# Kernel tuning notes

Hardware: AMD Instinct MI355X
Metric: run time of the kernel (lower is better)

The kernel has to match this reference:

```python
import jax, jax.numpy as jnp
import numpy as np

T, N, DEG = 8, 8192, 15
H = 4


def _gat(x, src, dst, wl, wr, a, b):
    """GATv2Conv with concat=False (heads averaged). x: [N, Cin] -> [N, Cout].
    e_ij = a_h . LeakyReLU(Wl x_j + Wr x_i); softmax over incoming edges of i;
    messages are Wl x_j (PyG GATv2 convention, self-loops already in edge list)."""
    n = x.shape[0]
    h, c = a.shape
    gl = (x @ wl).reshape(n, h, c)  # source-side transform
    gr = (x @ wr).reshape(n, h, c)  # target-side transform
    z = jax.nn.leaky_relu(gl[src] + gr[dst], 0.2)          # [E,H,C]
    e = jnp.einsum('ehc,hc->eh', z, a)                     # [E,H]
    m = jax.ops.segment_max(e, dst, num_segments=n)        # [N,H]
    ex = jnp.exp(e - m[dst])
    den = jax.ops.segment_sum(ex, dst, num_segments=n)     # [N,H]
    msg = jax.ops.segment_sum(ex[:, :, None] * gl[src], dst, num_segments=n)
    return (msg / den[:, :, None]).mean(axis=1) + b


def _d3(x, esrc, edst, wl, wr, a, b):
    # spatio-temporal graph conv: GATv2 applied independently per timestep
    return jax.lax.map(lambda args: _gat(args[0], args[1], args[2], wl, wr, a, b),
                       (x, esrc, edst))


def setup_inputs() -> dict:
    key = jax.random.key(0)
    ks = iter(jax.random.split(key, 32))
    x = jax.random.normal(next(ks), (T, N, 64), dtype=jnp.float32)
    # fixed-degree random graph per timestep + self loops (PyG add_self_loops=True)
    dst_base = jnp.repeat(jnp.arange(N, dtype=jnp.int32), DEG)
    src_r = jax.random.randint(next(ks), (T, N * DEG), 0, N, dtype=jnp.int32)
    loop = jnp.arange(N, dtype=jnp.int32)
    edge_src = jnp.concatenate([src_r, jnp.broadcast_to(loop, (T, N))], axis=1)
    edge_dst = jnp.concatenate([jnp.broadcast_to(dst_base, (T, N * DEG)),
                                jnp.broadcast_to(loop, (T, N))], axis=1)

    def gat_p(k, cin, cout):
        k1, k2, k3 = jax.random.split(k, 3)
        s = 1.0 / np.sqrt(cin)
        return ((jax.random.normal(k1, (cin, H * cout)) * s).astype(jnp.float32),
                (jax.random.normal(k2, (cin, H * cout)) * s).astype(jnp.float32),
                (jax.random.normal(k3, (H, cout)) * s).astype(jnp.float32),
                jnp.zeros((cout,), jnp.float32))

    inp = {"x": x, "edge_src": edge_src, "edge_dst": edge_dst}
    for name, cin, cout in [("c1", 64, 128), ("c2", 128, 64), ("c3", 64, 64), ("c4", 128, 64),
                            ("r11", 64, 64), ("r12", 64, 64), ("r2", 128, 128),
                            ("f11", 64, 64), ("f2", 128, 128)]:
        wl, wr, a, b = gat_p(next(ks), cin, cout)
        inp[name + "_wl"], inp[name + "_wr"], inp[name + "_a"], inp[name + "_b"] = wl, wr, a, b
    # ConvTranspose1d(k=1) == per-node linear conv_ch -> in_channels; then Linear in_channels -> original_dim
    for name, cin, cout in [("r3", 128, 64), ("f3", 128, 64), ("r4", 64, 64), ("f4", 64, 64)]:
        inp[name + "_w"] = (jax.random.normal(next(ks), (cin, cout)) * (1.0 / np.sqrt(cin))).astype(jnp.float32)
        inp[name + "_b"] = jnp.zeros((cout,), jnp.float32)
    return inp


def reference(x, edge_src, edge_dst,
              c1_wl, c1_wr, c1_a, c1_b, c2_wl, c2_wr, c2_a, c2_b,
              c3_wl, c3_wr, c3_a, c3_b, c4_wl, c4_wr, c4_a, c4_b,
              r11_wl, r11_wr, r11_a, r11_b, r12_wl, r12_wr, r12_a, r12_b,
              r2_wl, r2_wr, r2_a, r2_b, r3_w, r3_b, r4_w, r4_b,
              f11_wl, f11_wr, f11_a, f11_b, f2_wl, f2_wr, f2_a, f2_b,
              f3_w, f3_b, f4_w, f4_b):
    elu = jax.nn.elu
    out = elu(_d3(x, edge_src, edge_dst, c1_wl, c1_wr, c1_a, c1_b))           # [T,N,128]
    emb = elu(_d3(out, edge_src, edge_dst, c2_wl, c2_wr, c2_a, c2_b))         # [T,N,64]
    emb = elu(jnp.concatenate([_d3(emb, edge_src, edge_dst, c3_wl, c3_wr, c3_a, c3_b), emb], -1))  # [T,N,128]
    emb = elu(_d3(emb, edge_src, edge_dst, c4_wl, c4_wr, c4_a, c4_b))         # [T,N,64]

    # reconstruction branch on edges at t = -1
    s1, d1 = edge_src[-1], edge_dst[-1]
    r = elu(_gat(emb[-1], s1, d1, r11_wl, r11_wr, r11_a, r11_b))
    r = elu(jnp.concatenate([_gat(r, s1, d1, r12_wl, r12_wr, r12_a, r12_b), r], -1))  # [N,128]
    # F.dropout in eval mode -> identity
    r = elu(_gat(r, s1, d1, r2_wl, r2_wr, r2_a, r2_b))
    r = jnp.tanh(r @ r3_w + r3_b)
    recon = r @ r4_w + r4_b

    # forecasting branch on edges at t = -2 (original reuses reconstruct12 here)
    s2, d2 = edge_src[-2], edge_dst[-2]
    f = elu(_gat(emb[-2], s2, d2, f11_wl, f11_wr, f11_a, f11_b))
    f = elu(jnp.concatenate([_gat(f, s2, d2, r12_wl, r12_wr, r12_a, r12_b), f], -1))
    f = elu(_gat(f, s2, d2, f2_wl, f2_wr, f2_a, f2_b))
    f = jnp.tanh(f @ f3_w + f3_b)
    forecast = f @ f4_w + f4_b
    return (recon, forecast, emb)
```

## Files before the change

kernel.cpp:

```cpp
#include <hip/hip_runtime.h>
#include <cmath>

constexpr int T_   = 8;
constexpr int N_   = 8192;
constexpr int DEG_ = 15;
constexpr int E_   = N_ * (DEG_ + 1);
constexpr float L2E_ = 1.44269504f;

__device__ __forceinline__ float elu1(float v) {
  return v > 0.f ? v : exp2f(v * L2E_) - 1.f;
}

typedef __attribute__((ext_vector_type(8))) short bf16x8;
typedef __attribute__((ext_vector_type(4))) float f32x4;

__device__ __forceinline__ ushort f2bf(float x) {
  uint u = __float_as_uint(x);
  return (ushort)((u + 0x7FFFu + ((u >> 16) & 1u)) >> 16);
}
__device__ __forceinline__ float bf2f(ushort h) {
  return __uint_as_float(((uint)h) << 16);
}

template<int CTRL>
__device__ __forceinline__ float dpp_add(float x) {
  const int t = __builtin_amdgcn_mov_dpp(__float_as_int(x), CTRL, 0xf, 0xf, true);
  return x + __int_as_float(t);
}
__device__ __forceinline__ float row_reduce16(float x) {
  x = dpp_add<0x121>(x);
  x = dpp_add<0x122>(x);
  x = dpp_add<0x124>(x);
  x = dpp_add<0x128>(x);
  return x;
}

__global__ __launch_bounds__(256) void pad_edges(
    const int* __restrict__ es, uint* __restrict__ es16, int total)
{
  const int idx = blockIdx.x * 256 + threadIdx.x;
  if (idx >= total) return;
  const int t = idx >> 13, i = idx & (N_ - 1);
  const int* e = es + (size_t)t * E_ + (size_t)i * DEG_;
  uint o[16];
  #pragma unroll
  for (int k = 0; k < DEG_; k++) o[k] = (uint)e[k];
  o[15] = (uint)i;
  uint4* dst = (uint4*)(es16 + (size_t)idx * 16);
  dst[0] = make_uint4(o[0], o[1], o[2], o[3]);
  dst[1] = make_uint4(o[4], o[5], o[6], o[7]);
  dst[2] = make_uint4(o[8], o[9], o[10], o[11]);
  dst[3] = make_uint4(o[12], o[13], o[14], o[15]);
}

__global__ __launch_bounds__(256) void split_x(
    const float* __restrict__ X, ushort* __restrict__ XH, ushort* __restrict__ XL, int n4)
{
  const int i = blockIdx.x * 256 + threadIdx.x;
  if (i >= n4) return;
  const float4 v = ((const float4*)X)[i];
  const ushort h0 = f2bf(v.x), h1 = f2bf(v.y), h2 = f2bf(v.z), h3 = f2bf(v.w);
  ushort4 hh; hh.x = h0; hh.y = h1; hh.z = h2; hh.w = h3;
  ushort4 ll;
  ll.x = f2bf(v.x - bf2f(h0)); ll.y = f2bf(v.y - bf2f(h1));
  ll.z = f2bf(v.z - bf2f(h2)); ll.w = f2bf(v.w - bf2f(h3));
  ((ushort4*)XH)[i] = hh;
  ((ushort4*)XL)[i] = ll;
}

struct WTable {
  const float* wl[9]; const float* wr[9];
  int lgK[9]; int lgHC[9]; int off[9];
};
__global__ __launch_bounds__(256) void split_wt_all(
    WTable tb, ushort* __restrict__ WH, ushort* __restrict__ WL)
{
  const int y = blockIdx.y;
  const int lgK = tb.lgK[y], lgHC = tb.lgHC[y];
  const int n2 = 2 << (lgK + lgHC);
  const int idx = blockIdx.x * 256 + threadIdx.x;
  if (idx >= n2) return;
  const int k = idx & ((1 << lgK) - 1);
  const int n = (idx >> lgK) & ((1 << lgHC) - 1);
  const int s = idx >> (lgK + lgHC);
  const float* W = s ? tb.wr[y] : tb.wl[y];
  const float v = W[((size_t)k << lgHC) + n];
  const ushort h = f2bf(v);
  WH[tb.off[y] + idx] = h;
  WL[tb.off[y] + idx] = f2bf(v - bf2f(h));
}

__global__ __launch_bounds__(256) void gemm_mfma(
    const ushort* __restrict__ Ah, const ushort* __restrict__ Al,
    const ushort* __restrict__ Wh, const ushort* __restrict__ Wl,
    float* __restrict__ Cl, float* __restrict__ Cr,
    int M, int Ncol, int K, int nt)
{
  __shared__ alignas(16) ushort lAh[4 * 1032];
  __shared__ alignas(16) ushort lAl[4 * 1032];
  __shared__ alignas(16) ushort lBh[4 * 520];
  __shared__ alignas(16) ushort lBl[4 * 520];

  const int z = blockIdx.z;
  const int t = (z < nt) ? z : z - nt;
  const int side = (z < nt) ? 0 : 1;
  const ushort* __restrict__ Bh = Wh + (size_t)side * Ncol * K;
  const ushort* __restrict__ Bl = Wl + (size_t)side * Ncol * K;
  float* __restrict__ C = (side ? Cr : Cl) + (size_t)t * M * Ncol;
  const size_t aoff = (size_t)t * M * K;

  const int bm = blockIdx.x * 128, bn = blockIdx.y * 64;
  const int tid = threadIdx.x;
  const int wid = tid >> 6, lane = tid & 63;
  const int l15 = lane & 15, lk = lane >> 4;

  f32x4 acc[2][4] = {};

  for (int k0 = 0; k0 < K; k0 += 32) {
    #pragma unroll
    for (int c = 0; c < 2; c++) {
      const int ch = tid + c * 256;
      const int row = ch >> 2, kc = ch & 3;
      const size_t ga = aoff + (size_t)(bm + row) * K + (k0 + kc * 8);
      *(uint4*)&lAh[kc * 1032 + row * 8] = *(const uint4*)(Ah + ga);
      *(uint4*)&lAl[kc * 1032 + row * 8] = *(const uint4*)(Al + ga);
    }
    {
      const int col = tid >> 2, kc = tid & 3;
      const size_t gb = (size_t)(bn + col) * K + (k0 + kc * 8);
      *(uint4*)&lBh[kc * 520 + col * 8] = *(const uint4*)(Bh + gb);
      *(uint4*)&lBl[kc * 520 + col * 8] = *(const uint4*)(Bl + gb);
    }
    __syncthreads();

    bf16x8 ah[2], al[2], bh4[4], bl4[4];
    const int r0 = wid * 32;
    #pragma unroll
    for (int rf = 0; rf < 2; rf++) {
      const int ro = (r0 + rf * 16 + l15) * 8;
      ah[rf] = *(const bf16x8*)&lAh[lk * 1032 + ro];
      al[rf] = *(const bf16x8*)&lAl[lk * 1032 + ro];
    }
    #pragma unroll
    for (int cf = 0; cf < 4; cf++) {
      const int co = (cf * 16 + l15) * 8;
      bh4[cf] = *(const bf16x8*)&lBh[lk * 520 + co];
      bl4[cf] = *(const bf16x8*)&lBl[lk * 520 + co];
    }
    #pragma unroll
    for (int rf = 0; rf < 2; rf++)
      #pragma unroll
      for (int cf = 0; cf < 4; cf++) {
        acc[rf][cf] = __builtin_amdgcn_mfma_f32_16x16x32_bf16(ah[rf], bh4[cf], acc[rf][cf], 0, 0, 0);
        acc[rf][cf] = __builtin_amdgcn_mfma_f32_16x16x32_bf16(ah[rf], bl4[cf], acc[rf][cf], 0, 0, 0);
        acc[rf][cf] = __builtin_amdgcn_mfma_f32_16x16x32_bf16(al[rf], bh4[cf], acc[rf][cf], 0, 0, 0);
      }
    __syncthreads();
  }

  #pragma unroll
  for (int rf = 0; rf < 2; rf++)
    #pragma unroll
    for (int cf = 0; cf < 4; cf++) {
      const int col = bn + cf * 16 + l15;
      #pragma unroll
      for (int reg = 0; reg < 4; reg++) {
        const int row = bm + wid * 32 + rf * 16 + lk * 4 + reg;
        C[(size_t)row * Ncol + col] = acc[rf][cf][reg];
      }
    }
}

template<int EPI>
__global__ __launch_bounds__(256) void gemm_k(
    const float* __restrict__ A, const float* __restrict__ B,
    float* __restrict__ C, const float* __restrict__ bias,
    int M, int Ncol, int K)
{
  __shared__ float As[16][68];
  __shared__ float Bs[16][64];

  const int tid = threadIdx.x;
  const int tx = tid & 15, ty = tid >> 4;
  const int bm = blockIdx.x * 64, bn = blockIdx.y * 64;

  const int arow = tid >> 2;
  const int akc  = (tid & 3) * 4;
  const int brow = tid >> 4;
  const int bc4  = (tid & 15) * 4;

  float acc[4][4];
  #pragma unroll
  for (int i = 0; i < 4; i++)
    #pragma unroll
    for (int j = 0; j < 4; j++) acc[i][j] = 0.f;

  for (int k0 = 0; k0 < K; k0 += 16) {
    const float4 va = *(const float4*)(A + (size_t)(bm + arow) * K + (k0 + akc));
    const float4 vb = *(const float4*)(B + (size_t)(k0 + brow) * Ncol + (bn + bc4));
    As[akc + 0][arow] = va.x; As[akc + 1][arow] = va.y;
    As[akc + 2][arow] = va.z; As[akc + 3][arow] = va.w;
    *(float4*)&Bs[brow][bc4] = vb;
    __syncthreads();
    #pragma unroll
    for (int kk = 0; kk < 16; kk++) {
      const float4 av = *(const float4*)&As[kk][ty * 4];
      const float4 bv = *(const float4*)&Bs[kk][tx * 4];
      const float a4[4] = {av.x, av.y, av.z, av.w};
      const float b4[4] = {bv.x, bv.y, bv.z, bv.w};
      #pragma unroll
      for (int i = 0; i < 4; i++)
        #pragma unroll
        for (int j = 0; j < 4; j++)
          acc[i][j] = fmaf(a4[i], b4[j], acc[i][j]);
    }
    __syncthreads();
  }

  #pragma unroll
  for (int i = 0; i < 4; i++) {
    const int row = bm + ty * 4 + i;
    const int col = bn + tx * 4;
    float v[4] = {acc[i][0], acc[i][1], acc[i][2], acc[i][3]};
    #pragma unroll
    for (int j = 0; j < 4; j++) v[j] += bias[col + j];
    if (EPI == 1) {
      #pragma unroll
      for (int j = 0; j < 4; j++) v[j] = tanhf(v[j]);
    }
    *(float4*)(C + (size_t)row * Ncol + col) = make_float4(v[0], v[1], v[2], v[3]);
  }
}

template<bool SWZ, bool CONCAT, bool WF32>
__global__ __launch_bounds__(256) void gat_agg256(
    const float* __restrict__ GL, const float* __restrict__ GR,
    const float* __restrict__ aw_, const float* __restrict__ bias,
    const uint* __restrict__ es16, float* __restrict__ out,
    const float* __restrict__ csrc,
    ushort* __restrict__ SHo, ushort* __restrict__ SLo)
{
  constexpr int C = 64;
  constexpr int OSTR = CONCAT ? 128 : 64;

  const int lane = threadIdx.x & 63;
  const int wid  = threadIdx.x >> 6;
  const int bid  = blockIdx.x;
  const int t    = SWZ ? (bid & 7) : 0;
  const int ib   = SWZ ? (bid >> 3) : bid;
  const int gid  = t * N_ + ib * 4 + wid;

  const float* __restrict__ gl = GL + (size_t)t * N_ * 256;
  const uint*  __restrict__ ep = es16 + (size_t)gid * 16;
  const uint lo16 = (uint)lane << 4;

  float gr[4], a6[4], a4c[4];
  {
    const float4 gv = *(const float4*)(GR + (size_t)gid * 256 + lane * 4);
    const float4 av = *(const float4*)(aw_ + lane * 4);
    gr[0] = gv.x; gr[1] = gv.y; gr[2] = gv.z; gr[3] = gv.w;
    a6[0] = 0.6f * L2E_ * av.x; a6[1] = 0.6f * L2E_ * av.y;
    a6[2] = 0.6f * L2E_ * av.z; a6[3] = 0.6f * L2E_ * av.w;
    a4c[0] = 0.4f * L2E_ * av.x; a4c[1] = 0.4f * L2E_ * av.y;
    a4c[2] = 0.4f * L2E_ * av.z; a4c[3] = 0.4f * L2E_ * av.w;
  }

  float acc[4] = {0.f, 0.f, 0.f, 0.f};
  float den = 0.f, m = 0.f;

  #pragma unroll
  for (int b = 0; b < 4; b++) {
    const uint4 j4 = *(const uint4*)(ep + b * 4);
    uint off[4];
    off[0] = (j4.x << 10) + lo16;
    off[1] = (j4.y << 10) + lo16;
    off[2] = (j4.z << 10) + lo16;
    off[3] = (j4.w << 10) + lo16;
    float g[4][4];
    #pragma unroll
    for (int q = 0; q < 4; q++) {
      const float4 v = *(const float4*)((const char*)gl + off[q]);
      g[q][0] = v.x; g[q][1] = v.y; g[q][2] = v.z; g[q][3] = v.w;
    }
    float p[4];
    #pragma unroll
    for (int q = 0; q < 4; q++) {
      float s = 0.f;
      #pragma unroll
      for (int u = 0; u < 4; u++) {
        const float z = g[q][u] + gr[u];
        s = fmaf(z, a6[u], s);
        s = fmaf(fabsf(z), a4c[u], s);
      }
      p[q] = s;
    }
    #pragma unroll
    for (int q = 0; q < 4; q++) p[q] = row_reduce16(p[q]);

    const float bmax = fmaxf(fmaxf(p[0], p[1]), fmaxf(p[2], p[3]));
    if (b == 0) {
      m = bmax;
    } else {
      const float nm = fmaxf(m, bmax);
      const float sc = exp2f(m - nm);
      den *= sc;
      #pragma unroll
      for (int u = 0; u < 4; u++) acc[u] *= sc;
      m = nm;
    }
    #pragma unroll
    for (int q = 0; q < 4; q++) {
      const float w = exp2f(p[q] - m);
      den += w;
      #pragma unroll
      for (int u = 0; u < 4; u++) acc[u] = fmaf(w, g[q][u], acc[u]);
    }
  }

  const float inv = 0.25f / den;
  #pragma unroll
  for (int u = 0; u < 4; u++) acc[u] *= inv;
  #pragma unroll
  for (int u = 0; u < 4; u++) {
    acc[u] += __shfl_xor(acc[u], 16);
    acc[u] += __shfl_xor(acc[u], 32);
  }

  if (lane < 16) {
    float o[4];
    #pragma unroll
    for (int u = 0; u < 4; u++)
      o[u] = elu1(acc[u] + bias[lane * 4 + u]);
    if (WF32)
      *(float4*)(out + (size_t)gid * OSTR + lane * 4) = make_float4(o[0], o[1], o[2], o[3]);
    ushort4 hh, ll;
    hh.x = f2bf(o[0]); hh.y = f2bf(o[1]); hh.z = f2bf(o[2]); hh.w = f2bf(o[3]);
    ll.x = f2bf(o[0] - bf2f(hh.x)); ll.y = f2bf(o[1] - bf2f(hh.y));
    ll.z = f2bf(o[2] - bf2f(hh.z)); ll.w = f2bf(o[3] - bf2f(hh.w));
    *(ushort4*)(SHo + (size_t)gid * OSTR + lane * 4) = hh;
    *(ushort4*)(SLo + (size_t)gid * OSTR + lane * 4) = ll;
  } else if (CONCAT && lane < 32) {
    const int q = lane - 16;
    const float4 v = *(const float4*)(csrc + (size_t)gid * C + q * 4);
    const float o0 = elu1(v.x), o1 = elu1(v.y), o2 = elu1(v.z), o3 = elu1(v.w);
    if (WF32)
      *(float4*)(out + (size_t)gid * OSTR + C + q * 4) = make_float4(o0, o1, o2, o3);
    ushort4 hh, ll;
    hh.x = f2bf(o0); hh.y = f2bf(o1); hh.z = f2bf(o2); hh.w = f2bf(o3);
    ll.x = f2bf(o0 - bf2f(hh.x)); ll.y = f2bf(o1 - bf2f(hh.y));
    ll.z = f2bf(o2 - bf2f(hh.z)); ll.w = f2bf(o3 - bf2f(hh.w));
    *(ushort4*)(SHo + (size_t)gid * OSTR + C + q * 4) = hh;
    *(ushort4*)(SLo + (size_t)gid * OSTR + C + q * 4) = ll;
  }
}

template<bool SWZ, bool WF32, bool SPLIT>
__global__ __launch_bounds__(256) void gat_agg512(
    const float* __restrict__ GL, const float* __restrict__ GR,
    const float* __restrict__ aw_, const float* __restrict__ bias,
    const uint* __restrict__ es16, float* __restrict__ out,
    ushort* __restrict__ SHo, ushort* __restrict__ SLo)
{
  __shared__ float smem[4][128];

  const int lane = threadIdx.x & 63;
  const int h    = threadIdx.x >> 6;
  const int bid  = blockIdx.x;
  int t, i;
  if (SWZ) {
    const int xcd = bid & 7;
    t = xcd >> 1;
    i = ((bid >> 3) << 1) | (xcd & 1);
  } else {
    t = 0; i = bid;
  }
  const int gid = t * N_ + i;

  const float* __restrict__ gl = GL + (size_t)t * N_ * 512;
  const uint*  __restrict__ ep = es16 + (size_t)gid * 16;
  const int cb = h * 128 + lane * 2;
  const uint cbo = (uint)cb << 2;

  float gr0, gr1, a60, a61, a40, a41;
  {
    const float2 gv = *(const float2*)(GR + (size_t)gid * 512 + cb);
    const float2 av = *(const float2*)(aw_ + cb);
    gr0 = gv.x; gr1 = gv.y;
    a60 = 0.6f * L2E_ * av.x; a61 = 0.6f * L2E_ * av.y;
    a40 = 0.4f * L2E_ * av.x; a41 = 0.4f * L2E_ * av.y;
  }

  float acc0 = 0.f, acc1 = 0.f, den = 0.f, m = 0.f;

  #pragma unroll
  for (int b = 0; b < 4; b++) {
    const uint4 j4 = *(const uint4*)(ep + b * 4);
    uint off[4];
    off[0] = (j4.x << 11) + cbo;
    off[1] = (j4.y << 11) + cbo;
    off[2] = (j4.z << 11) + cbo;
    off[3] = (j4.w << 11) + cbo;
    float g[4][2];
    #pragma unroll
    for (int q = 0; q < 4; q++) {
      const float2 v = *(const float2*)((const char*)gl + off[q]);
      g[q][0] = v.x; g[q][1] = v.y;
    }
    float p[4];
    #pragma unroll
    for (int q = 0; q < 4; q++) {
      const float z0 = g[q][0] + gr0;
      const float z1 = g[q][1] + gr1;
      float s = z0 * a60;
      s = fmaf(fabsf(z0), a40, s);
      s = fmaf(z1, a61, s);
      s = fmaf(fabsf(z1), a41, s);
      p[q] = s;
    }
    #pragma unroll
    for (int q = 0; q < 4; q++) {
      p[q] = row_reduce16(p[q]);
      p[q] += __shfl_xor(p[q], 16);
      p[q] += __shfl_xor(p[q], 32);
    }
    const float bmax = fmaxf(fmaxf(p[0], p[1]), fmaxf(p[2], p[3]));
    if (b == 0) {
      m = bmax;
    } else {
      const float nm = fmaxf(m, bmax);
      const float sc = exp2f(m - nm);
      den *= sc; acc0 *= sc; acc1 *= sc;
      m = nm;
    }
    #pragma unroll
    for (int q = 0; q < 4; q++) {
      const float w = exp2f(p[q] - m);
      den += w;
      acc0 = fmaf(w, g[q][0], acc0);
      acc1 = fmaf(w, g[q][1], acc1);
    }
  }

  const float inv = 0.25f / den;
  smem[h][lane * 2]     = acc0 * inv;
  smem[h][lane * 2 + 1] = acc1 * inv;
  __syncthreads();

  if (h == 0) {
    const int c = lane * 2;
    float s0 = smem[0][c] + smem[1][c] + smem[2][c] + smem[3][c];
    float s1 = smem[0][c + 1] + smem[1][c + 1] + smem[2][c + 1] + smem[3][c + 1];
    s0 = elu1(s0 + bias[c]);
    s1 = elu1(s1 + bias[c + 1]);
    if (WF32)
      *(float2*)(out + (size_t)gid * 128 + c) = make_float2(s0, s1);
    if (SPLIT) {
      ushort2 hh, ll;
      hh.x = f2bf(s0); hh.y = f2bf(s1);
      ll.x = f2bf(s0 - bf2f(hh.x)); ll.y = f2bf(s1 - bf2f(hh.y));
      *(ushort2*)(SHo + (size_t)gid * 128 + c) = hh;
      *(ushort2*)(SLo + (size_t)gid * 128 + c) = ll;
    }
  }
}

extern "C" void kernel_launch(void* const* d_in, const int* in_sizes, int n_in,
                              void* d_out, int out_size, void* d_ws, size_t ws_size,
                              hipStream_t stream)
{
  (void)in_sizes; (void)n_in; (void)out_size; (void)ws_size;

  const float* x  = (const float*)d_in[0];
  const int*   es = (const int*)d_in[1];
  const float *c1_wl=(const float*)d_in[3], *c1_wr=(const float*)d_in[4], *c1_a=(const float*)d_in[5], *c1_b=(const float*)d_in[6];
  const float *c2_wl=(const float*)d_in[7], *c2_wr=(const float*)d_in[8], *c2_a=(const float*)d_in[9], *c2_b=(const float*)d_in[10];
  const float *c3_wl=(const float*)d_in[11],*c3_wr=(const float*)d_in[12],*c3_a=(const float*)d_in[13],*c3_b=(const float*)d_in[14];
  const float *c4_wl=(const float*)d_in[15],*c4_wr=(const float*)d_in[16],*c4_a=(const float*)d_in[17],*c4_b=(const float*)d_in[18];
  const float *r11_wl=(const float*)d_in[19],*r11_wr=(const float*)d_in[20],*r11_a=(const float*)d_in[21],*r11_b=(const float*)d_in[22];
  const float *r12_wl=(const float*)d_in[23],*r12_wr=(const float*)d_in[24],*r12_a=(const float*)d_in[25],*r12_b=(const float*)d_in[26];
  const float *r2_wl=(const float*)d_in[27],*r2_wr=(const float*)d_in[28],*r2_a=(const float*)d_in[29],*r2_b=(const float*)d_in[30];
  const float *f11_wl=(const float*)d_in[31],*f11_wr=(const float*)d_in[32],*f11_a=(const float*)d_in[33],*f11_b=(const float*)d_in[34];
  const float *f2_wl=(const float*)d_in[35],*f2_wr=(const float*)d_in[36],*f2_a=(const float*)d_in[37],*f2_b=(const float*)d_in[38];
  const float *r3_w=(const float*)d_in[39], *r3_b=(const float*)d_in[40];
  const float *f3_w=(const float*)d_in[41], *f3_b=(const float*)d_in[42];
  const float *r4_w=(const float*)d_in[43], *r4_b=(const float*)d_in[44];
  const float *f4_w=(const float*)d_in[45], *f4_b=(const float*)d_in[46];

  float* ws = (float*)d_ws;
  float* GL = ws;
  float* GR = GL + (size_t)16777216;
  float* A1 = GR + (size_t)16777216;
  float* B0 = A1 + (size_t)T_ * N_ * 64;
  float* B1 = B0 + (size_t)N_ * 128;
  ushort* SH  = (ushort*)(B1 + (size_t)N_ * 128);
  ushort* SL  = SH + (size_t)8388608;
  ushort* SH2 = SL + (size_t)8388608;
  ushort* SL2 = SH2 + (size_t)8388608;
  ushort* WH  = SL2 + (size_t)8388608;
  ushort* WL  = WH + (size_t)589824;
  uint*  ES16 = (uint*)(WL + (size_t)589824);

  float* recon = (float*)d_out;
  float* fcst  = recon + (size_t)N_ * 64;
  float* emb   = fcst + (size_t)N_ * 64;

  const dim3 blk(256);

  pad_edges<<<dim3(T_ * N_ / 256), blk, 0, stream>>>(es, ES16, T_ * N_);
  split_x<<<dim3(T_ * N_ * 64 / 4 / 256), blk, 0, stream>>>(x, SH, SL, T_ * N_ * 64 / 4);
  WTable tb;
  const float* wls[9] = {c1_wl, c2_wl, c3_wl, c4_wl, r11_wl, r12_wl, r2_wl, f11_wl, f2_wl};
  const float* wrs[9] = {c1_wr, c2_wr, c3_wr, c4_wr, r11_wr, r12_wr, r2_wr, f11_wr, f2_wr};
  const int Ks[9]  = {64, 128, 64, 128, 64, 64, 128, 64, 128};
  const int HCs[9] = {512, 256, 256, 256, 256, 256, 512, 256, 512};
  int woff[9]; int acc_off = 0;
  for (int y = 0; y < 9; y++) {
    tb.wl[y] = wls[y]; tb.wr[y] = wrs[y];
    tb.lgK[y] = __builtin_ctz(Ks[y]); tb.lgHC[y] = __builtin_ctz(HCs[y]);
    woff[y] = acc_off; tb.off[y] = acc_off;
    acc_off += 2 * Ks[y] * HCs[y];
  }
  split_wt_all<<<dim3(512, 9), blk, 0, stream>>>(tb, WH, WL);

  for (int ch = 0; ch < 2; ch++) {
    const int t0 = ch * 4, nt = 4;
    gemm_mfma<<<dim3(N_ / 128, 8, 2 * nt), blk, 0, stream>>>(
        SH + (size_t)t0 * N_ * 64, SL + (size_t)t0 * N_ * 64,
        WH + woff[0], WL + woff[0], GL, GR, N_, 512, 64, nt);
    gat_agg512<true, false, true><<<dim3(nt * N_), blk, 0, stream>>>(
        GL, GR, c1_a, c1_b, ES16 + (size_t)t0 * N_ * 16, nullptr,
        SH2 + (size_t)t0 * N_ * 128, SL2 + (size_t)t0 * N_ * 128);
  }
  gemm_mfma<<<dim3(N_ / 128, 4, 2 * T_), blk, 0, stream>>>(
      SH2, SL2, WH + woff[1], WL + woff[1], GL, GR, N_, 256, 128, T_);
  gat_agg256<true, false, true><<<dim3(T_ * N_ / 4), blk, 0, stream>>>(
      GL, GR, c2_a, c2_b, ES16, A1, nullptr, SH, SL);
  gemm_mfma<<<dim3(N_ / 128, 4, 2 * T_), blk, 0, stream>>>(
      SH, SL, WH + woff[2], WL + woff[2], GL, GR, N_, 256, 64, T_);
  gat_agg256<true, true, false><<<dim3(T_ * N_ / 4), blk, 0, stream>>>(
      GL, GR, c3_a, c3_b, ES16, nullptr, A1, SH, SL);
  gemm_mfma<<<dim3(N_ / 128, 4, 2 * T_), blk, 0, stream>>>(
      SH, SL, WH + woff[3], WL + woff[3], GL, GR, N_, 256, 128, T_);
  gat_agg256<true, false, true><<<dim3(T_ * N_ / 4), blk, 0, stream>>>(
      GL, GR, c4_a, c4_b, ES16, emb, nullptr, SH2, SL2);

  const uint* esR = ES16 + (size_t)7 * N_ * 16;
  gemm_mfma<<<dim3(N_ / 128, 4, 2), blk, 0, stream>>>(
      SH2 + (size_t)7 * N_ * 64, SL2 + (size_t)7 * N_ * 64,
      WH + woff[4], WL + woff[4], GL, GR, N_, 256, 64, 1);
  gat_agg256<false, false, true><<<dim3(N_ / 4), blk, 0, stream>>>(
      GL, GR, r11_a, r11_b, esR, B0, nullptr, SH, SL);
  gemm_mfma<<<dim3(N_ / 128, 4, 2), blk, 0, stream>>>(
      SH, SL, WH + woff[5], WL + woff[5], GL, GR, N_, 256, 64, 1);
  gat_agg256<false, true, false><<<dim3(N_ / 4), blk, 0, stream>>>(
      GL, GR, r12_a, r12_b, esR, nullptr, B0, SH, SL);
  gemm_mfma<<<dim3(N_ / 128, 8, 2), blk, 0, stream>>>(
      SH, SL, WH + woff[6], WL + woff[6], GL, GR, N_, 512, 128, 1);
  gat_agg512<false, true, false><<<dim3(N_), blk, 0, stream>>>(
      GL, GR, r2_a, r2_b, esR, B0, nullptr, nullptr);
  gemm_k<1><<<dim3(N_ / 64, 1, 1), blk, 0, stream>>>(B0, r3_w, B1, r3_b, N_, 64, 128);
  gemm_k<2><<<dim3(N_ / 64, 1, 1), blk, 0, stream>>>(B1, r4_w, recon, r4_b, N_, 64, 64);

  const uint* esF = ES16 + (size_t)6 * N_ * 16;
  gemm_mfma<<<dim3(N_ / 128, 4, 2), blk, 0, stream>>>(
      SH2 + (size_t)6 * N_ * 64, SL2 + (size_t)6 * N_ * 64,
      WH + woff[7], WL + woff[7], GL, GR, N_, 256, 64, 1);
  gat_agg256<false, false, true><<<dim3(N_ / 4), blk, 0, stream>>>(
      GL, GR, f11_a, f11_b, esF, B0, nullptr, SH, SL);
  gemm_mfma<<<dim3(N_ / 128, 4, 2), blk, 0, stream>>>(
      SH, SL, WH + woff[5], WL + woff[5], GL, GR, N_, 256, 64, 1);
  gat_agg256<false, true, false><<<dim3(N_ / 4), blk, 0, stream>>>(
      GL, GR, r12_a, r12_b, esF, nullptr, B0, SH, SL);
  gemm_mfma<<<dim3(N_ / 128, 8, 2), blk, 0, stream>>>(
      SH, SL, WH + woff[8], WL + woff[8], GL, GR, N_, 512, 128, 1);
  gat_agg512<false, true, false><<<dim3(N_), blk, 0, stream>>>(
      GL, GR, f2_a, f2_b, esF, B0, nullptr, nullptr);
  gemm_k<1><<<dim3(N_ / 64, 1, 1), blk, 0, stream>>>(B0, f3_w, B1, f3_b, N_, 64, 128);
  gemm_k<2><<<dim3(N_ / 64, 1, 1), blk, 0, stream>>>(B1, f4_w, fcst, f4_b, N_, 64, 64);
}
```

Measured before the change: 957.1 us.

## Batch recon and forecast branches into shared launches; write concat half in-place

The reconstruction (t=7) and forecasting (t=6) branches now run as single batched launches per layer, selecting per-timestep weights, attention vectors and biases by index. This halves the number of small launches and gives each grid twice as many blocks. The concat path no longer reads back a separate fp32 buffer. Instead the aggregation kernel writes the ELU'd copy of its own output into the second half of the bf16 split buffer, and the GEMM gains an lda parameter to read the wider rows. This drops the A1 intermediate buffer and its traffic, but makes the kernels more complex and relies on the hi/lo split staying consistent.

```diff
diff --git a/kernel.cpp b/kernel.cpp
--- a/kernel.cpp
+++ b/kernel.cpp
@@ -20,6 +20,14 @@
 }
 __device__ __forceinline__ float bf2f(ushort h) {
   return __uint_as_float(((uint)h) << 16);
+}
+__device__ __forceinline__ void wsplit4(ushort* SH, ushort* SL, size_t idx, const float* o) {
+  ushort4 hh, ll;
+  hh.x = f2bf(o[0]); hh.y = f2bf(o[1]); hh.z = f2bf(o[2]); hh.w = f2bf(o[3]);
+  ll.x = f2bf(o[0] - bf2f(hh.x)); ll.y = f2bf(o[1] - bf2f(hh.y));
+  ll.z = f2bf(o[2] - bf2f(hh.z)); ll.w = f2bf(o[3] - bf2f(hh.w));
+  *(ushort4*)(SH + idx) = hh;
+  *(ushort4*)(SL + idx) = ll;
 }
 
 template<int CTRL>
@@ -59,13 +67,8 @@
   const int i = blockIdx.x * 256 + threadIdx.x;
   if (i >= n4) return;
   const float4 v = ((const float4*)X)[i];
-  const ushort h0 = f2bf(v.x), h1 = f2bf(v.y), h2 = f2bf(v.z), h3 = f2bf(v.w);
-  ushort4 hh; hh.x = h0; hh.y = h1; hh.z = h2; hh.w = h3;
-  ushort4 ll;
-  ll.x = f2bf(v.x - bf2f(h0)); ll.y = f2bf(v.y - bf2f(h1));
-  ll.z = f2bf(v.z - bf2f(h2)); ll.w = f2bf(v.w - bf2f(h3));
-  ((ushort4*)XH)[i] = hh;
-  ((ushort4*)XL)[i] = ll;
+  const float o[4] = {v.x, v.y, v.z, v.w};
+  wsplit4(XH, XL, (size_t)i * 4, o);
 }
 
 struct WTable {
@@ -92,9 +95,9 @@
 
 __global__ __launch_bounds__(256) void gemm_mfma(
     const ushort* __restrict__ Ah, const ushort* __restrict__ Al,
-    const ushort* __restrict__ Wh, const ushort* __restrict__ Wl,
+    const ushort* __restrict__ WHb, const ushort* __restrict__ WLb,
     float* __restrict__ Cl, float* __restrict__ Cr,
-    int M, int Ncol, int K, int nt)
+    int M, int Ncol, int K, int lda, int nt, int woffA, int woffB)
 {
   __shared__ alignas(16) ushort lAh[4 * 1032];
   __shared__ alignas(16) ushort lAl[4 * 1032];
@@ -104,10 +107,11 @@
   const int z = blockIdx.z;
   const int t = (z < nt) ? z : z - nt;
   const int side = (z < nt) ? 0 : 1;
-  const ushort* __restrict__ Bh = Wh + (size_t)side * Ncol * K;
-  const ushort* __restrict__ Bl = Wl + (size_t)side * Ncol * K;
+  const int wo = (t == 1) ? woffB : woffA;
+  const ushort* __restrict__ Bh = WHb + wo + (size_t)side * Ncol * K;
+  const ushort* __restrict__ Bl = WLb + wo + (size_t)side * Ncol * K;
   float* __restrict__ C = (side ? Cr : Cl) + (size_t)t * M * Ncol;
-  const size_t aoff = (size_t)t * M * K;
+  const size_t aoff = (size_t)t * M * lda;
 
   const int bm = blockIdx.x * 128, bn = blockIdx.y * 64;
   const int tid = threadIdx.x;
@@ -121,7 +125,7 @@
     for (int c = 0; c < 2; c++) {
       const int ch = tid + c * 256;
       const int row = ch >> 2, kc = ch & 3;
-      const size_t ga = aoff + (size_t)(bm + row) * K + (k0 + kc * 8);
+      const size_t ga = aoff + (size_t)(bm + row) * lda + (k0 + kc * 8);
       *(uint4*)&lAh[kc * 1032 + row * 8] = *(const uint4*)(Ah + ga);
       *(uint4*)&lAl[kc * 1032 + row * 8] = *(const uint4*)(Al + ga);
     }
@@ -171,14 +175,20 @@
     }
 }
 
+struct GK2 {
+  const float* A[2]; const float* B[2]; float* C[2]; const float* bias[2];
+};
 template<int EPI>
-__global__ __launch_bounds__(256) void gemm_k(
-    const float* __restrict__ A, const float* __restrict__ B,
-    float* __restrict__ C, const float* __restrict__ bias,
-    int M, int Ncol, int K)
+__global__ __launch_bounds__(256) void gemm_k2(GK2 p, int M, int Ncol, int K)
 {
   __shared__ float As[16][68];
   __shared__ float Bs[16][64];
+
+  const int z = blockIdx.z;
+  const float* __restrict__ A = p.A[z];
+  const float* __restrict__ B = p.B[z];
+  float* __restrict__ C = p.C[z];
+  const float* __restrict__ bias = p.bias[z];
 
   const int tid = threadIdx.x;
   const int tx = tid & 15, ty = tid >> 4;
@@ -232,23 +242,22 @@
   }
 }
 
-template<bool SWZ, bool CONCAT, bool WF32>
+template<bool SWZ, bool BATCH2, bool DUP, bool WF32, int OSTR>
 __global__ __launch_bounds__(256) void gat_agg256(
     const float* __restrict__ GL, const float* __restrict__ GR,
-    const float* __restrict__ aw_, const float* __restrict__ bias,
+    const float* __restrict__ aw0, const float* __restrict__ aw1,
+    const float* __restrict__ b0, const float* __restrict__ b1,
     const uint* __restrict__ es16, float* __restrict__ out,
-    const float* __restrict__ csrc,
     ushort* __restrict__ SHo, ushort* __restrict__ SLo)
 {
-  constexpr int C = 64;
-  constexpr int OSTR = CONCAT ? 128 : 64;
-
   const int lane = threadIdx.x & 63;
   const int wid  = threadIdx.x >> 6;
   const int bid  = blockIdx.x;
-  const int t    = SWZ ? (bid & 7) : 0;
-  const int ib   = SWZ ? (bid >> 3) : bid;
+  const int t    = SWZ ? (bid & 7) : (BATCH2 ? (bid >> 11) : 0);
+  const int ib   = SWZ ? (bid >> 3) : (BATCH2 ? (bid & 2047) : bid);
   const int gid  = t * N_ + ib * 4 + wid;
+  const float* __restrict__ aw_  = (BATCH2 && t == 1) ? aw1 : aw0;
+  const float* __restrict__ bias = (BATCH2 && t == 1) ? b1 : b0;
 
   const float* __restrict__ gl = GL + (size_t)t * N_ * 256;
   const uint*  __restrict__ ep = es16 + (size_t)gid * 16;
@@ -333,31 +342,22 @@
       o[u] = elu1(acc[u] + bias[lane * 4 + u]);
     if (WF32)
       *(float4*)(out + (size_t)gid * OSTR + lane * 4) = make_float4(o[0], o[1], o[2], o[3]);
-    ushort4 hh, ll;
-    hh.x = f2bf(o[0]); hh.y = f2bf(o[1]); hh.z = f2bf(o[2]); hh.w = f2bf(o[3]);
-    ll.x = f2bf(o[0] - bf2f(hh.x)); ll.y = f2bf(o[1] - bf2f(hh.y));
-    ll.z = f2bf(o[2] - bf2f(hh.z)); ll.w = f2bf(o[3] - bf2f(hh.w));
-    *(ushort4*)(SHo + (size_t)gid * OSTR + lane * 4) = hh;
-    *(ushort4*)(SLo + (size_t)gid * OSTR + lane * 4) = ll;
-  } else if (CONCAT && lane < 32) {
+    wsplit4(SHo, SLo, (size_t)gid * OSTR + lane * 4, o);
+  } else if (DUP && lane < 32) {
     const int q = lane - 16;
-    const float4 v = *(const float4*)(csrc + (size_t)gid * C + q * 4);
-    const float o0 = elu1(v.x), o1 = elu1(v.y), o2 = elu1(v.z), o3 = elu1(v.w);
-    if (WF32)
-      *(float4*)(out + (size_t)gid * OSTR + C + q * 4) = make_float4(o0, o1, o2, o3);
-    ushort4 hh, ll;
-    hh.x = f2bf(o0); hh.y = f2bf(o1); hh.z = f2bf(o2); hh.w = f2bf(o3);
-    ll.x = f2bf(o0 - bf2f(hh.x)); ll.y = f2bf(o1 - bf2f(hh.y));
-    ll.z = f2bf(o2 - bf2f(hh.z)); ll.w = f2bf(o3 - bf2f(hh.w));
-    *(ushort4*)(SHo + (size_t)gid * OSTR + C + q * 4) = hh;
-    *(ushort4*)(SLo + (size_t)gid * OSTR + C + q * 4) = ll;
-  }
-}
-
-template<bool SWZ, bool WF32, bool SPLIT>
+    float o[4];
+    #pragma unroll
+    for (int u = 0; u < 4; u++)
+      o[u] = elu1(elu1(acc[u] + bias[q * 4 + u]));
+    wsplit4(SHo, SLo, (size_t)gid * OSTR + 64 + q * 4, o);
+  }
+}
+
+template<bool SWZ, bool BATCH2, bool WF32, bool SPLIT>
 __global__ __launch_bounds__(256) void gat_agg512(
     const float* __restrict__ GL, const float* __restrict__ GR,
-    const float* __restrict__ aw_, const float* __restrict__ bias,
+    const float* __restrict__ aw0, const float* __restrict__ aw1,
+    const float* __restrict__ b0, const float* __restrict__ b1,
     const uint* __restrict__ es16, float* __restrict__ out,
     ushort* __restrict__ SHo, ushort* __restrict__ SLo)
 {
@@ -371,10 +371,14 @@
     const int xcd = bid & 7;
     t = xcd >> 1;
     i = ((bid >> 3) << 1) | (xcd & 1);
+  } else if (BATCH2) {
+    t = bid >> 13; i = bid & (N_ - 1);
   } else {
     t = 0; i = bid;
   }
   const int gid = t * N_ + i;
+  const float* __restrict__ aw_  = (BATCH2 && t == 1) ? aw1 : aw0;
+  const float* __restrict__ bias = (BATCH2 && t == 1) ? b1 : b0;
 
   const float* __restrict__ gl = GL + (size_t)t * N_ * 512;
   const uint*  __restrict__ ep = es16 + (size_t)gid * 16;
@@ -489,10 +493,9 @@
   float* ws = (float*)d_ws;
   float* GL = ws;
   float* GR = GL + (size_t)16777216;
-  float* A1 = GR + (size_t)16777216;
-  float* B0 = A1 + (size_t)T_ * N_ * 64;
-  float* B1 = B0 + (size_t)N_ * 128;
-  ushort* SH  = (ushort*)(B1 + (size_t)N_ * 128);
+  float* B0 = GR + (size_t)16777216;
+  float* B1 = B0 + (size_t)2 * N_ * 128;
+  ushort* SH  = (ushort*)(B1 + (size_t)2 * N_ * 64);
   ushort* SL  = SH + (size_t)8388608;
   ushort* SH2 = SL + (size_t)8388608;
   ushort* SL2 = SH2 + (size_t)8388608;
@@ -526,55 +529,48 @@
     const int t0 = ch * 4, nt = 4;
     gemm_mfma<<<dim3(N_ / 128, 8, 2 * nt), blk, 0, stream>>>(
         SH + (size_t)t0 * N_ * 64, SL + (size_t)t0 * N_ * 64,
-        WH + woff[0], WL + woff[0], GL, GR, N_, 512, 64, nt);
-    gat_agg512<true, false, true><<<dim3(nt * N_), blk, 0, stream>>>(
-        GL, GR, c1_a, c1_b, ES16 + (size_t)t0 * N_ * 16, nullptr,
+        WH, WL, GL, GR, N_, 512, 64, 64, nt, woff[0], woff[0]);
+    gat_agg512<true, false, false, true><<<dim3(nt * N_), blk, 0, stream>>>(
+        GL, GR, c1_a, c1_a, c1_b, c1_b, ES16 + (size_t)t0 * N_ * 16, nullptr,
         SH2 + (size_t)t0 * N_ * 128, SL2 + (size_t)t0 * N_ * 128);
   }
   gemm_mfma<<<dim3(N_ / 128, 4, 2 * T_), blk, 0, stream>>>(
-      SH2, SL2, WH + woff[1], WL + woff[1], GL, GR, N_, 256, 128, T_);
-  gat_agg256<true, false, true><<<dim3(T_ * N_ / 4), blk, 0, stream>>>(
-      GL, GR, c2_a, c2_b, ES16, A1, nullptr, SH, SL);
+      SH2, SL2, WH, WL, GL, GR, N_, 256, 128, 128, T_, woff[1], woff[1]);
+  gat_agg256<true, false, true, false, 128><<<dim3(T_ * N_ / 4), blk, 0, stream>>>(
+      GL, GR, c2_a, c2_a, c2_b, c2_b, ES16, nullptr, SH, SL);
   gemm_mfma<<<dim3(N_ / 128, 4, 2 * T_), blk, 0, stream>>>(
-      SH, SL, WH + woff[2], WL + woff[2], GL, GR, N_, 256, 64, T_);
-  gat_agg256<true, true, false><<<dim3(T_ * N_ / 4), blk, 0, stream>>>(
-      GL, GR, c3_a, c3_b, ES16, nullptr, A1, SH, SL);
+      SH, SL, WH, WL, GL, GR, N_, 256, 64, 128, T_, woff[2], woff[2]);
+  gat_agg256<true, false, false, false, 128><<<dim3(T_ * N_ / 4), blk, 0, stream>>>(
+      GL, GR, c3_a, c3_a, c3_b, c3_b, ES16, nullptr, SH, SL);
   gemm_mfma<<<dim3(N_ / 128, 4, 2 * T_), blk, 0, stream>>>(
-      SH, SL, WH + woff[3], WL + woff[3], GL, GR, N_, 256, 128, T_);
-  gat_agg256<true, false, true><<<dim3(T_ * N_ / 4), blk, 0, stream>>>(
-      GL, GR, c4_a, c4_b, ES16, emb, nullptr, SH2, SL2);
-
-  const uint* esR = ES16 + (size_t)7 * N_ * 16;
-  gemm_mfma<<<dim3(N_ / 128, 4, 2), blk, 0, stream>>>(
-      SH2 + (size_t)7 * N_ * 64, SL2 + (size_t)7 * N_ * 64,
-      WH + woff[4], WL + woff[4], GL, GR, N_, 256, 64, 1);
-  gat_agg256<false, false, true><<<dim3(N_ / 4), blk, 0, stream>>>(
-      GL, GR, r11_a, r11_b, esR, B0, nullptr, SH, SL);
-  gemm_mfma<<<dim3(N_ / 128, 4, 2), blk, 0, stream>>>(
-      SH, SL, WH + woff[5], WL + woff[5], GL, GR, N_, 256, 64, 1);
-  gat_agg256<false, true, false><<<dim3(N_ / 4), blk, 0, stream>>>(
-      GL, GR, r12_a, r12_b, esR, nullptr, B0, SH, SL);
-  gemm_mfma<<<dim3(N_ / 128, 8, 2), blk, 0, stream>>>(
-      SH, SL, WH + woff[6], WL + woff[6], GL, GR, N_, 512, 128, 1);
-  gat_agg512<false, true, false><<<dim3(N_), blk, 0, stream>>>(
-      GL, GR, r2_a, r2_b, esR, B0, nullptr, nullptr);
-  gemm_k<1><<<dim3(N_ / 64, 1, 1), blk, 0, stream>>>(B0, r3_w, B1, r3_b, N_, 64, 128);
-  gemm_k<2><<<dim3(N_ / 64, 1, 1), blk, 0, stream>>>(B1, r4_w, recon, r4_b, N_, 64, 64);
-
-  const uint* esF = ES16 + (size_t)6 * N_ * 16;
-  gemm_mfma<<<dim3(N_ / 128, 4, 2), blk, 0, stream>>>(
+      SH, SL, WH, WL, GL, GR, N_, 256, 128, 128, T_, woff[3], woff[3]);
+  gat_agg256<true, false, false, true, 64><<<dim3(T_ * N_ / 4), blk, 0, stream>>>(
+      GL, GR, c4_a, c4_a, c4_b, c4_b, ES16, emb, SH2, SL2);
+
+  const uint* esB = ES16 + (size_t)6 * N_ * 16;
+  gemm_mfma<<<dim3(N_ / 128, 4, 4), blk, 0, stream>>>(
       SH2 + (size_t)6 * N_ * 64, SL2 + (size_t)6 * N_ * 64,
-      WH + woff[7], WL + woff[7], GL, GR, N_, 256, 64, 1);
-  gat_agg256<false, false, true><<<dim3(N_ / 4), blk, 0, stream>>>(
-      GL, GR, f11_a, f11_b, esF, B0, nullptr, SH, SL);
-  gemm_mfma<<<dim3(N_ / 128, 4, 2), blk, 0, stream>>>(
-      SH, SL, WH + woff[5], WL + woff[5], GL, GR, N_, 256, 64, 1);
-  gat_agg256<false, true, false><<<dim3(N_ / 4), blk, 0, stream>>>(
-      GL, GR, r12_a, r12_b, esF, nullptr, B0, SH, SL);
-  gemm_mfma<<<dim3(N_ / 128, 8, 2), blk, 0, stream>>>(
-      SH, SL, WH + woff[8], WL + woff[8], GL, GR, N_, 512, 128, 1);
-  gat_agg512<false, true, false><<<dim3(N_), blk, 0, stream>>>(
-      GL, GR, f2_a, f2_b, esF, B0, nullptr, nullptr);
-  gemm_k<1><<<dim3(N_ / 64, 1, 1), blk, 0, stream>>>(B0, f3_w, B1, f3_b, N_, 64, 128);
-  gemm_k<2><<<dim3(N_ / 64, 1, 1), blk, 0, stream>>>(B1, f4_w, fcst, f4_b, N_, 64, 64);
-}
+      WH, WL, GL, GR, N_, 256, 64, 64, 2, woff[7], woff[4]);
+  gat_agg256<false, true, true, false, 128><<<dim3(2 * N_ / 4), blk, 0, stream>>>(
+      GL, GR, f11_a, r11_a, f11_b, r11_b, esB, nullptr, SH, SL);
+  gemm_mfma<<<dim3(N_ / 128, 4, 4), blk, 0, stream>>>(
+      SH, SL, WH, WL, GL, GR, N_, 256, 64, 128, 2, woff[5], woff[5]);
+  gat_agg256<false, true, false, false, 128><<<dim3(2 * N_ / 4), blk, 0, stream>>>(
+      GL, GR, r12_a, r12_a, r12_b, r12_b, esB, nullptr, SH, SL);
+  gemm_mfma<<<dim3(N_ / 128, 8, 4), blk, 0, stream>>>(
+      SH, SL, WH, WL, GL, GR, N_, 512, 128, 128, 2, woff[8], woff[6]);
+  gat_agg512<false, true, true, false><<<dim3(2 * N_), blk, 0, stream>>>(
+      GL, GR, f2_a, r2_a, f2_b, r2_b, esB, B0, nullptr, nullptr);
+  GK2 p3;
+  p3.A[0] = B0; p3.A[1] = B0 + (size_t)N_ * 128;
+  p3.B[0] = f3_w; p3.B[1] = r3_w;
+  p3.C[0] = B1; p3.C[1] = B1 + (size_t)N_ * 64;
+  p3.bias[0] = f3_b; p3.bias[1] = r3_b;
+  gemm_k2<1><<<dim3(N_ / 64, 1, 2), blk, 0, stream>>>(p3, N_, 64, 128);
+  GK2 p4;
+  p4.A[0] = B1; p4.A[1] = B1 + (size_t)N_ * 64;
+  p4.B[0] = f4_w; p4.B[1] = r4_w;
+  p4.C[0] = fcst; p4.C[1] = recon;
+  p4.bias[0] = f4_b; p4.bias[1] = r4_b;
+  gemm_k2<2><<<dim3(N_ / 64, 1, 2), blk, 0, stream>>>(p4, N_, 64, 64);
+}
```

Measured after the change: 905.2 us. -5.4%, faster.
